# Performance work log

Hardware: AMD Instinct MI355X
Metric: run time of the kernel (lower is better)

## Reference

```python
import jax, jax.numpy as jnp
import numpy as np

EPS_LN = 1e-12
EPS_BN = 1e-5


def layernorm(x, w, b):
    u = jnp.mean(x, axis=-1, keepdims=True)
    s = jnp.mean((x - u) ** 2, axis=-1, keepdims=True)
    return w * ((x - u) / jnp.sqrt(s + EPS_LN)) + b


def reps_block(x, ln1_w, ln1_b, lin_w, lin_b, ln2_w, ln2_b):
    # GRAPHLayerNorm -> (dropout, identity in eval) -> Linear -> ReLU -> GRAPHLayerNorm
    h = layernorm(x, ln1_w, ln1_b)
    h = jax.nn.relu(jnp.einsum('bnd,od->bno', h, lin_w) + lin_b)
    return layernorm(h, ln2_w, ln2_b)


def attend(x):
    # full dense self-attention: softmax(x x^T) x ; dropout is identity in eval
    scores = jnp.einsum('bnd,bmd->bnm', x, x)  # [B,4096,4096]
    attn = jax.nn.softmax(scores, axis=-1)
    return jnp.einsum('bnm,bmd->bnd', attn, x)


def setup_inputs() -> dict:
    key = jax.random.key(0)
    ks = jax.random.split(key, 8)
    B, C, H, W = 4, 512, 64, 64
    D = 512
    inp = {
        'T1': jax.random.normal(ks[0], (B, C, H, W), jnp.float32),
        'T2': jax.random.normal(ks[1], (B, C, H, W), jnp.float32),
        'w_conv3': jax.random.normal(ks[2], (1024, 1024, 3, 3), jnp.float32) * 0.01,
        'w_conv1': jax.random.normal(ks[3], (512, 1024, 1, 1), jnp.float32) * 0.03,
        'bn_gamma': jnp.ones((512,), jnp.float32),
        'bn_beta': jnp.zeros((512,), jnp.float32),
        'bn_mean': jnp.zeros((512,), jnp.float32),
        'bn_var': jnp.ones((512,), jnp.float32),
        'ln1_w': jnp.ones((D,), jnp.float32),
        'ln1_b': jnp.zeros((D,), jnp.float32),
        'lin_w': jax.random.normal(ks[4], (D, D), jnp.float32) * 0.04,
        'lin_b': jnp.zeros((D,), jnp.float32),
        'ln2_w': jnp.ones((D,), jnp.float32),
        'ln2_b': jnp.zeros((D,), jnp.float32),
    }
    return inp


def reference(T1, T2, w_conv3, w_conv1, bn_gamma, bn_beta, bn_mean, bn_var,
              ln1_w, ln1_b, lin_w, lin_b, ln2_w, ln2_b):
    B = T1.shape[0]
    X = jnp.concatenate((T1, T2), axis=1)  # [B,1024,64,64]
    dn = ('NCHW', 'OIHW', 'NCHW')
    X = jax.lax.conv_general_dilated(X, w_conv3, (1, 1), ((1, 1), (1, 1)), dimension_numbers=dn)
    X = jax.lax.conv_general_dilated(X, w_conv1, (1, 1), ((0, 0), (0, 0)), dimension_numbers=dn)  # [B,512,64,64]
    # BatchNorm (eval, running stats) + ReLU
    inv = (bn_gamma / jnp.sqrt(bn_var + EPS_BN))[None, :, None, None]
    X = jax.nn.relu(X * inv + (bn_beta - bn_mean * bn_gamma / jnp.sqrt(bn_var + EPS_BN))[None, :, None, None])
    x = X.transpose(0, 2, 3, 1).reshape(B, 4096, 512)
    # block 1
    rel = attend(x)
    rel = reps_block(x + rel, ln1_w, ln1_b, lin_w, lin_b, ln2_w, ln2_b)
    # block 2 (original code reuses self.reps_graph, i.e. SAME params)
    rel1 = attend(rel)
    rel1 = reps_block(rel + rel1, ln1_w, ln1_b, lin_w, lin_b, ln2_w, ln2_b)
    return rel1.reshape(B, 64, 64, 512).transpose(0, 3, 1, 2)  # [B,512,64,64]
```

## Files before the change

kernel.cpp:

```cpp
#include <hip/hip_runtime.h>
#include <stdint.h>

typedef float f32x4 __attribute__((ext_vector_type(4)));
typedef __bf16 bf16x8 __attribute__((ext_vector_type(8)));
typedef unsigned short u16;
typedef unsigned short u16x8 __attribute__((ext_vector_type(8)));

__device__ __forceinline__ float bf2f(u16 u){ unsigned int i = ((unsigned int)u)<<16; float f; __builtin_memcpy(&f,&i,4); return f; }
__device__ __forceinline__ u16 f2bf(float f){ unsigned int i; __builtin_memcpy(&i,&f,4); i += 0x7FFFu + ((i>>16)&1u); return (u16)(i>>16); }
__device__ __forceinline__ u16 f2h(float f){ _Float16 h = (_Float16)f; u16 b; __builtin_memcpy(&b,&h,2); return b; }
__device__ __forceinline__ float h2f(u16 b){ _Float16 h; __builtin_memcpy(&h,&b,2); return (float)h; }

__device__ __forceinline__ void gld16(const void* g, void* l){
  __builtin_amdgcn_global_load_lds(
      (const __attribute__((address_space(1))) void*)(uintptr_t)g,
      (__attribute__((address_space(3))) void*)(unsigned int)(uintptr_t)l, 16, 0, 0);
}

__global__ __launch_bounds__(256) void pad_interior(const float* __restrict__ T1,
                                                    const float* __restrict__ T2,
                                                    u16* __restrict__ Xpad){
  const int n = blockIdx.z, ct = blockIdx.y, pt = blockIdx.x;
  const int t = threadIdx.x;
  const int c0 = ct*64, p0 = pt*64;
  const float* src = (c0 < 512) ? (T1 + ((long)n*512 + c0)*4096)
                                : (T2 + ((long)n*512 + (c0-512))*4096);
  __shared__ u16 lds[64][66];
  #pragma unroll
  for (int i=0;i<4;i++){
    int c = i*16 + (t>>4);
    int ch = t&15;
    float4 v = *(const float4*)(src + (long)c*4096 + p0 + ch*4);
    int p = ch*4;
    lds[p+0][c] = f2bf(v.x); lds[p+1][c] = f2bf(v.y);
    lds[p+2][c] = f2bf(v.z); lds[p+3][c] = f2bf(v.w);
  }
  __syncthreads();
  #pragma unroll
  for (int i=0;i<8;i++){
    int p = i*8 + (t>>5);
    int c2 = t&31;
    int pix = p0 + p; int yy = (pix>>6)+1, xx = (pix&63)+1;
    ushort2 val; val.x = lds[p][2*c2]; val.y = lds[p][2*c2+1];
    *(ushort2*)(Xpad + (((long)n*66 + yy)*66 + xx)*1024 + c0 + 2*c2) = val;
  }
}

__global__ __launch_bounds__(256) void prep_w3(const float* __restrict__ w3, u16* __restrict__ wk3t){
  const int o = blockIdx.x; const int t = threadIdx.x;
  __shared__ u16 lds[9216];
  const float* src = w3 + (long)o*9216;
  #pragma unroll
  for (int i=0;i<9;i++){
    int j = i*256 + t;
    float4 v = *(const float4*)(src + j*4);
    lds[j*4+0]=f2bf(v.x); lds[j*4+1]=f2bf(v.y); lds[j*4+2]=f2bf(v.z); lds[j*4+3]=f2bf(v.w);
  }
  __syncthreads();
  u16* dst = wk3t + (long)o*9216;
  #pragma unroll
  for (int i=0;i<36;i++){
    int j = i*256 + t; int tp = j>>10, ci = j&1023;
    dst[j] = lds[ci*9+tp];
  }
}

__global__ void prep_small(const float* __restrict__ w1, const float* __restrict__ bg,
                           const float* __restrict__ bb, const float* __restrict__ bm,
                           const float* __restrict__ bv, const float* __restrict__ linw,
                           u16* __restrict__ w1t, u16* __restrict__ lint,
                           float* __restrict__ bias1){
  const int b = blockIdx.x, t = threadIdx.x;
  if (b < 2048){
    long i = (long)b*256 + t;
    int o = (int)(i>>10);
    float inv = bg[o] / sqrtf(bv[o] + 1e-5f);
    w1t[i] = f2bf(w1[i]*inv);
  } else if (b < 3072){
    long i = (long)(b-2048)*256 + t;
    lint[i] = f2bf(linw[i]);
  } else {
    int o = (b-3072)*256 + t;
    float inv = bg[o]/sqrtf(bv[o]+1e-5f);
    bias1[o] = bb[o] - bm[o]*inv;
  }
}

__global__ __launch_bounds__(256) void row_norm(const u16* __restrict__ x, float* __restrict__ nrm){
  const int row = blockIdx.x*4 + (threadIdx.x>>6);
  const int lane = threadIdx.x & 63;
  u16x8 q = *(const u16x8*)(x + (long)row*512 + lane*8);
  float s = 0.f;
  #pragma unroll
  for (int j=0;j<8;j++){ float f = bf2f(q[j]); s += f*f; }
  #pragma unroll
  for (int off=32; off; off>>=1) s += __shfl_xor(s, off);
  if (lane==0) nrm[row] = s;
}

__global__ __launch_bounds__(256) void transpose_bf(const u16* __restrict__ src, u16* __restrict__ dst,
                                                    int R, int C, long sStr, long dStr){
  const int z = blockIdx.z;
  src += (long)z*sStr; dst += (long)z*dStr;
  const int r0 = blockIdx.x*64, c0 = blockIdx.y*64;
  const int t = threadIdx.x;
  __shared__ u16 lds[64][66];
  #pragma unroll
  for (int i=0;i<4;i++){
    int r = i*16 + (t>>4), ch = t&15;
    ushort4 v = *(const ushort4*)(src + (long)(r0+r)*C + c0 + ch*4);
    lds[r][ch*4+0]=v.x; lds[r][ch*4+1]=v.y; lds[r][ch*4+2]=v.z; lds[r][ch*4+3]=v.w;
  }
  __syncthreads();
  #pragma unroll
  for (int i=0;i<4;i++){
    int c = i*16 + (t>>4), ch = t&15;
    ushort4 v;
    v.x = lds[ch*4+0][c]; v.y = lds[ch*4+1][c]; v.z = lds[ch*4+2][c]; v.w = lds[ch*4+3][c];
    *(ushort4*)(dst + (long)(c0+c)*R + r0 + ch*4) = v;
  }
}

__global__ __launch_bounds__(256) void transpose_bf_f32(const u16* __restrict__ src, float* __restrict__ dst){
  const int z = blockIdx.z;
  src += (long)z*4096*512; dst += (long)z*512*4096;
  const int r0 = blockIdx.x*64, c0 = blockIdx.y*64;
  const int t = threadIdx.x;
  __shared__ u16 lds[64][66];
  #pragma unroll
  for (int i=0;i<4;i++){
    int r = i*16 + (t>>4), ch = t&15;
    ushort4 v = *(const ushort4*)(src + (long)(r0+r)*512 + c0 + ch*4);
    lds[r][ch*4+0]=v.x; lds[r][ch*4+1]=v.y; lds[r][ch*4+2]=v.z; lds[r][ch*4+3]=v.w;
  }
  __syncthreads();
  #pragma unroll
  for (int i=0;i<4;i++){
    int c = i*16 + (t>>4), ch = t&15;
    float4 v;
    v.x = bf2f(lds[ch*4+0][c]); v.y = bf2f(lds[ch*4+1][c]);
    v.z = bf2f(lds[ch*4+2][c]); v.w = bf2f(lds[ch*4+3][c]);
    *(float4*)(dst + (long)(c0+c)*4096 + r0 + ch*4) = v;
  }
}

template<int EPI, int CONV>
__global__ __launch_bounds__(512, 2) void gemm256(
    const u16* __restrict__ Ain, const u16* __restrict__ Btin, void* __restrict__ Cv,
    int K, int lda, int ldb, int ldc, const float* __restrict__ srowIn,
    u16* __restrict__ C0, u16* __restrict__ C1, u16* __restrict__ C2, u16* __restrict__ C3)
{
  extern __shared__ u16 sm[];
  const int t = threadIdx.x;
  const int lane = t & 63;
  const int wid = t >> 6;
  const int wr = wid >> 2, wc = wid & 3;

  long m0, n0;
  int byv = 0, bxv = 0;
  const u16* A; const u16* Bt; const float* srow; u16* Cz;
  if (EPI == 3){
    const int orig = blockIdx.x;
    const int swz = (orig & 7) * 68 + (orig >> 3);
    const int z = swz / 136;
    int p = swz % 136;
    int by = 0;
    while (p >= 16 - by){ p -= 16 - by; by++; }
    const int bx = by + p;
    byv = by; bxv = bx;
    m0 = (long)by * 256; n0 = (long)bx * 256;
    A = Ain + (long)z*4096*lda;
    Bt = A;
    srow = srowIn + (long)z*4096;
    Cz = (z==0)?C0:(z==1)?C1:(z==2)?C2:C3;
  } else {
    const int orig = blockIdx.y * gridDim.x + blockIdx.x;
    const int cpx = (gridDim.x * gridDim.y) >> 3;
    const int swz = (orig & 7) * cpx + (orig >> 3);
    const int bx = swz % gridDim.x;
    const int by = swz / gridDim.x;
    m0 = (long)by * 256; n0 = (long)bx * 256;
    A = Ain; Bt = Btin; srow = srowIn; Cz = (u16*)Cv;
  }

  const int row0 = t >> 2;
  const int cs0  = (t & 3) ^ ((row0 >> 1) & 3);

  const u16 *aB0, *aB1;
  if (CONV) {
    long m_ = m0 + row0;
    long pb0 = ((long)((int)(m_>>12)*66 + (int)((m_>>6)&63)))*66 + (int)(m_&63);
    m_ = m0 + row0 + 128;
    long pb1 = ((long)((int)(m_>>12)*66 + (int)((m_>>6)&63)))*66 + (int)(m_&63);
    aB0 = A + pb0*1024 + cs0*8;
    aB1 = A + pb1*1024 + cs0*8;
  } else {
    aB0 = A + (m0 + row0)*(long)lda + cs0*8;
    aB1 = A + (m0 + row0 + 128)*(long)lda + cs0*8;
  }
  const u16* bB0 = Bt + (n0 + row0)*(long)ldb + cs0*8;
  const u16* bB1 = Bt + (n0 + row0 + 128)*(long)ldb + cs0*8;

  auto issueA = [&](int sub, long aoff){
    u16* d = sm + sub*8192 + t*8;
    gld16(aB0 + aoff, d);
    gld16(aB1 + aoff, d + 4096);
  };
  auto issueB = [&](int sub, long boff){
    u16* d = sm + 32768 + sub*8192 + t*8;
    gld16(bB0 + boff, d);
    gld16(bB1 + boff, d + 4096);
  };
  auto conv_aoff = [&](int tile)->long {
    int kb = tile << 6;
    int tap = kb >> 10;
    int cb  = kb & 1023;
    int ky = (tap >= 6) ? 2 : (tap >= 3 ? 1 : 0);
    int kx = tap - ky*3;
    return (long)(ky*66 + kx)*1024 + cb;
  };

  const int frow = lane & 15;
  const int elemoff = (((lane>>4) ^ ((frow>>1)&3)) << 3);
  const int rAoff = (wr*128 + frow)*32 + elemoff;
  const int rBoff = (wc*64  + frow)*32 + elemoff;

  f32x4 acc[8][4] = {};

  {
    long a0 = CONV ? conv_aoff(0) : 0L;
    issueA(0, a0);
    issueB(0, 0);
    issueA(1, a0 + 32);
    issueB(1, 32);
  }

  const int NT = K >> 6;
  for (int tile = 0; tile < NT; ++tile) {
    const int b = tile & 1;
    const int nb2 = b ^ 1;
    const bool lastT = (tile == NT-1);
    long aoffN = 0, boffN = 0;
    if (!lastT) {
      aoffN = CONV ? conv_aoff(tile+1) : (long)(tile+1)*64;
      boffN = (long)(tile+1)*64;
    }

    asm volatile("s_waitcnt vmcnt(4)" ::: "memory");
    __builtin_amdgcn_s_barrier();
    __builtin_amdgcn_sched_barrier(0);

    {
      const u16* pA = sm + (b*2+0)*8192 + rAoff;
      const u16* pB = sm + 32768 + (b*2+0)*8192 + rBoff;
      bf16x8 bf[4];
      #pragma unroll
      for (int i=0;i<4;i++) bf[i] = *(const bf16x8*)(pB + i*512);
      {
        bf16x8 a[4];
        #pragma unroll
        for (int i=0;i<4;i++) a[i] = *(const bf16x8*)(pA + i*512);
        if (!lastT) issueA(nb2*2+0, aoffN);
        __builtin_amdgcn_s_setprio(1);
        #pragma unroll
        for (int mi=0;mi<4;mi++)
          #pragma unroll
          for (int ni=0;ni<4;ni++)
            acc[mi][ni] = __builtin_amdgcn_mfma_f32_16x16x32_bf16(a[mi], bf[ni], acc[mi][ni],0,0,0);
        __builtin_amdgcn_s_setprio(0);
      }
      {
        bf16x8 a[4];
        #pragma unroll
        for (int i=0;i<4;i++) a[i] = *(const bf16x8*)(pA + (4+i)*512);
        if (!lastT) issueB(nb2*2+0, boffN);
        __builtin_amdgcn_s_setprio(1);
        #pragma unroll
        for (int mi=0;mi<4;mi++)
          #pragma unroll
          for (int ni=0;ni<4;ni++)
            acc[4+mi][ni] = __builtin_amdgcn_mfma_f32_16x16x32_bf16(a[mi], bf[ni], acc[4+mi][ni],0,0,0);
        __builtin_amdgcn_s_setprio(0);
      }
    }

    if (lastT) asm volatile("s_waitcnt vmcnt(0)" ::: "memory");
    else       asm volatile("s_waitcnt vmcnt(4)" ::: "memory");
    __builtin_amdgcn_s_barrier();
    __builtin_amdgcn_sched_barrier(0);

    {
      const u16* pA = sm + (b*2+1)*8192 + rAoff;
      const u16* pB = sm + 32768 + (b*2+1)*8192 + rBoff;
      bf16x8 bf[4];
      #pragma unroll
      for (int i=0;i<4;i++) bf[i] = *(const bf16x8*)(pB + i*512);
      {
        bf16x8 a[4];
        #pragma unroll
        for (int i=0;i<4;i++) a[i] = *(const bf16x8*)(pA + i*512);
        if (!lastT) issueA(nb2*2+1, aoffN + 32);
        __builtin_amdgcn_s_setprio(1);
        #pragma unroll
        for (int mi=0;mi<4;mi++)
          #pragma unroll
          for (int ni=0;ni<4;ni++)
            acc[mi][ni] = __builtin_amdgcn_mfma_f32_16x16x32_bf16(a[mi], bf[ni], acc[mi][ni],0,0,0);
        __builtin_amdgcn_s_setprio(0);
      }
      {
        bf16x8 a[4];
        #pragma unroll
        for (int i=0;i<4;i++) a[i] = *(const bf16x8*)(pA + (4+i)*512);
        if (!lastT) issueB(nb2*2+1, boffN + 32);
        __builtin_amdgcn_s_setprio(1);
        #pragma unroll
        for (int mi=0;mi<4;mi++)
          #pragma unroll
          for (int ni=0;ni<4;ni++)
            acc[4+mi][ni] = __builtin_amdgcn_mfma_f32_16x16x32_bf16(a[mi], bf[ni], acc[4+mi][ni],0,0,0);
        __builtin_amdgcn_s_setprio(0);
      }
    }
  }

  const int crow0 = wr*128 + ((lane>>4)<<2);
  const int ccol0 = wc*64 + frow;

  #pragma unroll
  for (int mi=0;mi<8;mi++){
    #pragma unroll
    for (int ni=0;ni<4;ni++){
      long col = n0 + ccol0 + ni*16;
      #pragma unroll
      for (int r=0;r<4;r++){
        long row = m0 + crow0 + mi*16 + r;
        float v = acc[mi][ni][r];
        if (EPI==3) Cz[row*(long)ldc + col] = f2h(v - srow[row]);
        else        Cz[row*(long)ldc + col] = f2bf(v);
      }
    }
  }

  if (EPI == 3 && bxv != byv){
    __syncthreads();
    u16* lt = sm;
    float sc[4];
    #pragma unroll
    for (int ni=0;ni<4;ni++) sc[ni] = srow[n0 + ccol0 + ni*16];
    #pragma unroll
    for (int mi=0;mi<8;mi++){
      const int g = (crow0 + mi*16) >> 2;
      #pragma unroll
      for (int ni=0;ni<4;ni++){
        const int col_l = ccol0 + ni*16;
        ushort4 pk;
        #pragma unroll
        for (int r=0;r<4;r++) pk[r] = f2h(acc[mi][ni][r] - sc[ni]);
        *(ushort4*)(lt + col_l*256 + ((g ^ (col_l & 63))<<2)) = pk;
      }
    }
    __syncthreads();
    const int half = lane >> 5, l32 = lane & 31;
    #pragma unroll
    for (int ps=0; ps<16; ps++){
      const int R = ps*16 + wid*2 + half;
      const int u0 = ((l32<<1)    ) ^ (R & 63);
      const int u1 = ((l32<<1) | 1) ^ (R & 63);
      ushort4 a = *(const ushort4*)(lt + R*256 + (u0<<2));
      ushort4 b = *(const ushort4*)(lt + R*256 + (u1<<2));
      u16* dst = Cz + (n0 + R)*(long)ldc + m0 + (l32<<3);
      *(ushort4*)dst = a;
      *(ushort4*)(dst+4) = b;
    }
  }
}

template<int EPI>
__global__ __launch_bounds__(256, 2) void gemm_bt(
    const u16* __restrict__ A, const u16* __restrict__ Bt,
    void* __restrict__ Cv, const float* __restrict__ bias,
    int K, int lda, int ldb, int ldc)
{
  const int t = threadIdx.x;
  const int lane = t & 63;
  const int w = t >> 6;
  const int wr = w >> 1, wc = w & 1;
  const long m0 = (long)blockIdx.y * 128;
  const long n0 = (long)blockIdx.x * 128;

  __shared__ u16 lA[128*32];
  __shared__ u16 lB[128*32];

  const u16* aS0 = A + (m0 + (t>>2))*(long)lda + (t&3)*8;
  const u16* aS1 = aS0 + 64*(long)lda;
  const u16* bS0 = Bt + (n0 + (t>>2))*(long)ldb + (t&3)*8;
  const u16* bS1 = bS0 + 64*(long)ldb;
  u16* dA0 = lA + t*8; u16* dA1 = lA + 2048 + t*8;
  u16* dB0 = lB + t*8; u16* dB1 = lB + 2048 + t*8;

  f32x4 acc[4][4] = {};
  const int frow = lane & 15, kq = (lane >> 4) * 8;
  const u16* rA = lA + (wr*64 + frow)*32 + kq;
  const u16* rB = lB + (wc*64 + frow)*32 + kq;

  for (int kb = 0; kb < K; kb += 32) {
    gld16(aS0 + kb, dA0); gld16(aS1 + kb, dA1);
    gld16(bS0 + kb, dB0); gld16(bS1 + kb, dB1);
    __syncthreads();
    bf16x8 af[4], bfr[4];
    #pragma unroll
    for (int i=0;i<4;i++) af[i]  = *(const bf16x8*)(rA + i*512);
    #pragma unroll
    for (int i=0;i<4;i++) bfr[i] = *(const bf16x8*)(rB + i*512);
    #pragma unroll
    for (int mi=0;mi<4;mi++)
      #pragma unroll
      for (int ni=0;ni<4;ni++)
        acc[mi][ni] = __builtin_amdgcn_mfma_f32_16x16x32_bf16(af[mi], bfr[ni], acc[mi][ni], 0,0,0);
    __syncthreads();
  }

  const int crow0 = wr*64 + ((lane>>4)<<2);
  const int ccol0 = wc*64 + (lane&15);
  #pragma unroll
  for (int mi=0;mi<4;mi++){
    #pragma unroll
    for (int ni=0;ni<4;ni++){
      long col = n0 + ccol0 + ni*16;
      float bv = (EPI==1) ? bias[col] : 0.0f;
      #pragma unroll
      for (int r=0;r<4;r++){
        long row = m0 + crow0 + mi*16 + r;
        float v = acc[mi][ni][r];
        if (EPI==1){ v += bv; v = v > 0.0f ? v : 0.0f; }
        ((u16*)Cv)[row*(long)ldc + col] = f2bf(v);
      }
    }
  }
}

__global__ __launch_bounds__(256, 2) void pv5(
    const u16* __restrict__ P0, const u16* __restrict__ P1,
    const u16* __restrict__ P2, const u16* __restrict__ P3,
    const u16* __restrict__ xT, u16* __restrict__ attb)
{
  extern __shared__ u16 pm[];
  const int L = blockIdx.x;
  const int xcd = L & 7;
  const int z = xcd >> 1;
  const int tile = ((L >> 3) << 1) + (xcd & 1);
  const int bx = tile & 3, by = tile >> 2;
  const long ZS = 4096L*512;
  const u16* A  = (z==0)?P0:(z==1)?P1:(z==2)?P2:P3;
  const u16* Bt = xT   + (long)z*ZS;
  u16*       C  = attb + (long)z*ZS;
  const long m0 = (long)by * 128, n0 = (long)bx * 128;

  const int t = threadIdx.x;
  const int lane = t & 63;
  const int w = t >> 6;
  const int wr = w >> 1, wc = w & 1;

  const int row0 = t >> 2;
  const int cs0  = (t & 3) ^ ((row0 >> 1) & 3);

  const u16* aB0 = A + (m0 + row0)*4096L + cs0*8;
  const u16* aB1 = aB0 + 64*4096L;
  const u16* bB0 = Bt + (n0 + row0)*4096L + cs0*8;
  const u16* bB1 = bB0 + 64*4096L;

  auto issueA = [&](int sub, long off){
    u16* d = pm + sub*4096 + t*8;
    gld16(aB0 + off, d);
    gld16(aB1 + off, d + 2048);
  };
  auto issueB = [&](int sub, long off){
    u16* d = pm + 16384 + sub*4096 + t*8;
    gld16(bB0 + off, d);
    gld16(bB1 + off, d + 2048);
  };

  const int frow = lane & 15;
  const int elemoff = (((lane>>4) ^ ((frow>>1)&3)) << 3);
  const int rAoff = (wr*64 + frow)*32 + elemoff;
  const int rBoff = (wc*64 + frow)*32 + elemoff;

  f32x4 acc[4][4] = {};

  issueA(0, 0);  issueB(0, 0);
  issueA(1, 32); issueB(1, 32);

  const int NT = 64;
  for (int tl = 0; tl < NT; ++tl) {
    const int b = tl & 1;
    const int nb2 = b ^ 1;
    const bool lastT = (tl == NT-1);
    const long offN = (long)(tl+1)*64;

    asm volatile("s_waitcnt vmcnt(4)" ::: "memory");
    __builtin_amdgcn_s_barrier();
    __builtin_amdgcn_sched_barrier(0);

    {
      const u16* pA = pm + (b*2+0)*4096 + rAoff;
      const u16* pB = pm + 16384 + (b*2+0)*4096 + rBoff;
      bf16x8 bf[4];
      #pragma unroll
      for (int i=0;i<4;i++) bf[i] = *(const bf16x8*)(pB + i*512);
      {
        bf16x8 a[2];
        #pragma unroll
        for (int i=0;i<2;i++) a[i] = *(const bf16x8*)(pA + i*512);
        if (!lastT) issueA(nb2*2+0, offN);
        __builtin_amdgcn_s_setprio(1);
        #pragma unroll
        for (int mi=0;mi<2;mi++)
          #pragma unroll
          for (int ni=0;ni<4;ni++)
            acc[mi][ni] = __builtin_amdgcn_mfma_f32_16x16x32_bf16(a[mi], bf[ni], acc[mi][ni],0,0,0);
        __builtin_amdgcn_s_setprio(0);
      }
      {
        bf16x8 a[2];
        #pragma unroll
        for (int i=0;i<2;i++) a[i] = *(const bf16x8*)(pA + (2+i)*512);
        if (!lastT) issueB(nb2*2+0, offN);
        __builtin_amdgcn_s_setprio(1);
        #pragma unroll
        for (int mi=0;mi<2;mi++)
          #pragma unroll
          for (int ni=0;ni<4;ni++)
            acc[2+mi][ni] = __builtin_amdgcn_mfma_f32_16x16x32_bf16(a[mi], bf[ni], acc[2+mi][ni],0,0,0);
        __builtin_amdgcn_s_setprio(0);
      }
    }

    if (lastT) asm volatile("s_waitcnt vmcnt(0)" ::: "memory");
    else       asm volatile("s_waitcnt vmcnt(4)" ::: "memory");
    __builtin_amdgcn_s_barrier();
    __builtin_amdgcn_sched_barrier(0);

    {
      const u16* pA = pm + (b*2+1)*4096 + rAoff;
      const u16* pB = pm + 16384 + (b*2+1)*4096 + rBoff;
      bf16x8 bf[4];
      #pragma unroll
      for (int i=0;i<4;i++) bf[i] = *(const bf16x8*)(pB + i*512);
      {
        bf16x8 a[2];
        #pragma unroll
        for (int i=0;i<2;i++) a[i] = *(const bf16x8*)(pA + i*512);
        if (!lastT) issueA(nb2*2+1, offN + 32);
        __builtin_amdgcn_s_setprio(1);
        #pragma unroll
        for (int mi=0;mi<2;mi++)
          #pragma unroll
          for (int ni=0;ni<4;ni++)
            acc[mi][ni] = __builtin_amdgcn_mfma_f32_16x16x32_bf16(a[mi], bf[ni], acc[mi][ni],0,0,0);
        __builtin_amdgcn_s_setprio(0);
      }
      {
        bf16x8 a[2];
        #pragma unroll
        for (int i=0;i<2;i++) a[i] = *(const bf16x8*)(pA + (2+i)*512);
        if (!lastT) issueB(nb2*2+1, offN + 32);
        __builtin_amdgcn_s_setprio(1);
        #pragma unroll
        for (int mi=0;mi<2;mi++)
          #pragma unroll
          for (int ni=0;ni<4;ni++)
            acc[2+mi][ni] = __builtin_amdgcn_mfma_f32_16x16x32_bf16(a[mi], bf[ni], acc[2+mi][ni],0,0,0);
        __builtin_amdgcn_s_setprio(0);
      }
    }
  }

  const int crow0 = wr*64 + ((lane>>4)<<2);
  const int ccol0 = wc*64 + frow;
  #pragma unroll
  for (int mi=0;mi<4;mi++){
    #pragma unroll
    for (int ni=0;ni<4;ni++){
      long col = n0 + ccol0 + ni*16;
      #pragma unroll
      for (int r=0;r<4;r++){
        long row = m0 + crow0 + mi*16 + r;
        C[row*512 + col] = f2bf(acc[mi][ni][r]);
      }
    }
  }
}

__global__ __launch_bounds__(256) void softmax_batched(
    u16* __restrict__ S0, u16* __restrict__ S1,
    u16* __restrict__ S2, u16* __restrict__ S3)
{
  const int z = blockIdx.x >> 12;
  const long row = blockIdx.x & 4095;
  u16* buf = (z==0)?S0:(z==1)?S1:(z==2)?S2:S3;
  u16* src = buf + row*4096;
  const int t = threadIdx.x, lane = t&63, w = t>>6;
  float v[16];
  #pragma unroll
  for (int i=0;i<2;i++){
    u16x8 q = *(const u16x8*)(src + t*16 + i*8);
    #pragma unroll
    for (int j=0;j<8;j++) v[i*8+j] = h2f(q[j]);
  }
  float mx = v[0];
  #pragma unroll
  for (int i=1;i<16;i++) mx = fmaxf(mx, v[i]);
  #pragma unroll
  for (int off=32; off; off>>=1) mx = fmaxf(mx, __shfl_xor(mx, off));
  __shared__ float red[4];
  if (lane==0) red[w] = mx;
  __syncthreads();
  mx = fmaxf(fmaxf(red[0],red[1]), fmaxf(red[2],red[3]));
  float sum = 0.0f;
  #pragma unroll
  for (int i=0;i<16;i++){ v[i] = __expf(v[i]-mx); sum += v[i]; }
  #pragma unroll
  for (int off=32; off; off>>=1) sum += __shfl_xor(sum, off);
  __shared__ float red2[4];
  if (lane==0) red2[w] = sum;
  __syncthreads();
  sum = red2[0]+red2[1]+red2[2]+red2[3];
  const float inv = 1.0f/sum;
  #pragma unroll
  for (int i=0;i<2;i++){
    u16x8 o;
    #pragma unroll
    for (int j=0;j<8;j++) o[j] = f2bf(v[i*8+j]*inv);
    *(u16x8*)(src + t*16 + i*8) = o;
  }
}

template<int ADD>
__global__ __launch_bounds__(256) void ln_row(
    const u16* __restrict__ X, const u16* __restrict__ Y,
    const float* __restrict__ w, const float* __restrict__ b,
    u16* __restrict__ outB)
{
  const long row = blockIdx.x;
  const int t = threadIdx.x, lane = t&63, wv = t>>6;
  ushort2 xv = *(const ushort2*)(X + row*512 + t*2);
  float v0 = bf2f(xv.x), v1 = bf2f(xv.y);
  if (ADD){
    ushort2 yv = *(const ushort2*)(Y + row*512 + t*2);
    v0 += bf2f(yv.x); v1 += bf2f(yv.y);
  }
  float s = v0+v1, q = v0*v0 + v1*v1;
  #pragma unroll
  for (int off=32; off; off>>=1){ s += __shfl_xor(s,off); q += __shfl_xor(q,off); }
  __shared__ float red[8];
  if (lane==0){ red[wv]=s; red[4+wv]=q; }
  __syncthreads();
  s = red[0]+red[1]+red[2]+red[3];
  q = red[4]+red[5]+red[6]+red[7];
  const float u = s*(1.0f/512.0f);
  const float var = q*(1.0f/512.0f) - u*u;
  const float inv = rsqrtf(var + 1e-12f);
  const int c = t*2;
  float o0 = (v0-u)*inv*w[c]   + b[c];
  float o1 = (v1-u)*inv*w[c+1] + b[c+1];
  ushort2 ov; ov.x=f2bf(o0); ov.y=f2bf(o1);
  *(ushort2*)(outB + row*512 + c) = ov;
}

extern "C" void kernel_launch(void* const* d_in, const int* in_sizes, int n_in,
                              void* d_out, int out_size, void* d_ws, size_t ws_size,
                              hipStream_t stream) {
  const float* T1   = (const float*)d_in[0];
  const float* T2   = (const float*)d_in[1];
  const float* w3   = (const float*)d_in[2];
  const float* w1   = (const float*)d_in[3];
  const float* bg   = (const float*)d_in[4];
  const float* bb   = (const float*)d_in[5];
  const float* bm   = (const float*)d_in[6];
  const float* bv   = (const float*)d_in[7];
  const float* ln1w = (const float*)d_in[8];
  const float* ln1b = (const float*)d_in[9];
  const float* linw = (const float*)d_in[10];
  const float* linb = (const float*)d_in[11];
  const float* ln2w = (const float*)d_in[12];
  const float* ln2b = (const float*)d_in[13];

  hipFuncSetAttribute(reinterpret_cast<const void*>(gemm256<0,1>),
                      hipFuncAttributeMaxDynamicSharedMemorySize, 131072);
  hipFuncSetAttribute(reinterpret_cast<const void*>(gemm256<3,0>),
                      hipFuncAttributeMaxDynamicSharedMemorySize, 131072);
  hipFuncSetAttribute(reinterpret_cast<const void*>(pv5),
                      hipFuncAttributeMaxDynamicSharedMemorySize, 65536);

  char* ws = (char*)d_ws;
  size_t off = 0;
  auto alloc = [&](size_t bytes)->char* {
    char* p = ws + off;
    off += (bytes + 255) & ~(size_t)255;
    return p;
  };
  const size_t XPAD_B = 4L*66*66*1024*2;
  u16*   Xpad  = (u16*)  alloc(XPAD_B);
  u16*   wk3t  = (u16*)  alloc(1024L*9216*2);
  u16*   w1t   = (u16*)  alloc(512L*1024*2);
  u16*   lint  = (u16*)  alloc(512L*512*2);
  float* bias1 = (float*)alloc(512*4);
  float* nrm   = (float*)alloc(16384L*4);
  u16*   Y1    = (u16*)  alloc(16384L*1024*2);
  u16*   x0    = (u16*)  alloc(16384L*512*2);
  u16*   xT    = (u16*)  alloc(4L*512*4096*2);
  u16*   Sreg  = (u16*)  alloc(2L*4096*4096*2);
  u16*   attb  = (u16*)  alloc(16384L*512*2);
  u16*   h     = (u16*)  alloc(16384L*512*2);
  u16*   g     = (u16*)  alloc(16384L*512*2);
  u16*   rel1  = (u16*)  alloc(16384L*512*2);
  u16*   S0    = Y1;
  u16*   S1    = Sreg;
  u16*   S2    = Sreg + 4096L*4096;
  u16*   S3    = Xpad;
  if (off > ws_size) return;

  const long ZS = 4096L*512;

  hipMemsetAsync(Xpad, 0, XPAD_B, stream);
  pad_interior<<<dim3(64,16,4), 256, 0, stream>>>(T1, T2, Xpad);
  prep_w3<<<1024, 256, 0, stream>>>(w3, wk3t);
  prep_small<<<3074, 256, 0, stream>>>(w1, bg, bb, bm, bv, linw, w1t, lint, bias1);

  gemm256<0,1><<<dim3(4,64), 512, 131072, stream>>>(Xpad, wk3t, (void*)Y1, 9216, 0, 9216, 1024,
                                                    nullptr, nullptr, nullptr, nullptr, nullptr);
  gemm_bt<1><<<dim3(4,128), 256, 0, stream>>>(Y1, w1t, (void*)x0, bias1, 1024, 1024, 1024, 512);

  auto attend = [&](const u16* xin){
    transpose_bf<<<dim3(64,8,4), 256, 0, stream>>>(xin, xT, 4096, 512, ZS, ZS);
    row_norm<<<4096, 256, 0, stream>>>(xin, nrm);
    gemm256<3,0><<<dim3(544), 512, 131072, stream>>>(xin, xin, nullptr, 512, 512, 512, 4096,
                                                     nrm, S0, S1, S2, S3);
    softmax_batched<<<16384, 256, 0, stream>>>(S0, S1, S2, S3);
    pv5<<<512, 256, 65536, stream>>>(S0, S1, S2, S3, xT, attb);
  };

  attend(x0);
  ln_row<1><<<16384, 256, 0, stream>>>(x0, attb, ln1w, ln1b, h);
  gemm_bt<1><<<dim3(4,128), 256, 0, stream>>>(h, lint, (void*)g, linb, 512, 512, 512, 512);
  ln_row<0><<<16384, 256, 0, stream>>>(g, nullptr, ln2w, ln2b, rel1);

  attend(rel1);
  ln_row<1><<<16384, 256, 0, stream>>>(rel1, attb, ln1w, ln1b, h);
  gemm_bt<1><<<dim3(4,128), 256, 0, stream>>>(h, lint, (void*)g, linb, 512, 512, 512, 512);
  ln_row<0><<<16384, 256, 0, stream>>>(g, nullptr, ln2w, ln2b, x0);

  transpose_bf_f32<<<dim3(64,8,4), 256, 0, stream>>>(x0, (float*)d_out);
}
```

Baseline: 814.5 us.

## Replace simple 128x128 GEMM with deep-pipelined swizzled LDS GEMM and XCD-aware tile mapping

Replaces the single-buffered gemm_bt, which synchronised twice per 32-wide K step, with gemm128_deep. The new kernel double-buffers two 32-wide K sub-tiles in dynamic LDS, issues the next loads between MFMA groups, and uses vmcnt waits with s_setprio. It also XOR-swizzles the LDS layout to reduce bank conflicts and remaps block indices so tiles are grouped per XCD for L2 locality. pv5's tile mapping is changed as well. The cost is more LDS per block (64KB), which may limit occupancy, and hand-scheduled waits that are fragile.

```diff
diff --git a/kernel.cpp b/kernel.cpp
--- a/kernel.cpp
+++ b/kernel.cpp
@@ -377,52 +377,139 @@
 }
 
 template<int EPI>
-__global__ __launch_bounds__(256, 2) void gemm_bt(
-    const u16* __restrict__ A, const u16* __restrict__ Bt,
-    void* __restrict__ Cv, const float* __restrict__ bias,
-    int K, int lda, int ldb, int ldc)
+__global__ __launch_bounds__(256, 2) void gemm128_deep(
+    const u16* __restrict__ A, const u16* __restrict__ Bt, u16* __restrict__ C,
+    const float* __restrict__ bias, int K, int lda, int ldb, int ldc)
 {
+  extern __shared__ u16 pm[];
+  const int L = blockIdx.x;
+  const int xcd = L & 7;
+  const int q = L >> 3;
+  const int by = (q >> 2) + xcd*16;
+  const int bx = q & 3;
+  const long m0 = (long)by * 128, n0 = (long)bx * 128;
+
   const int t = threadIdx.x;
   const int lane = t & 63;
   const int w = t >> 6;
   const int wr = w >> 1, wc = w & 1;
-  const long m0 = (long)blockIdx.y * 128;
-  const long n0 = (long)blockIdx.x * 128;
-
-  __shared__ u16 lA[128*32];
-  __shared__ u16 lB[128*32];
-
-  const u16* aS0 = A + (m0 + (t>>2))*(long)lda + (t&3)*8;
-  const u16* aS1 = aS0 + 64*(long)lda;
-  const u16* bS0 = Bt + (n0 + (t>>2))*(long)ldb + (t&3)*8;
-  const u16* bS1 = bS0 + 64*(long)ldb;
-  u16* dA0 = lA + t*8; u16* dA1 = lA + 2048 + t*8;
-  u16* dB0 = lB + t*8; u16* dB1 = lB + 2048 + t*8;
+
+  const int row0 = t >> 2;
+  const int cs0  = (t & 3) ^ ((row0 >> 1) & 3);
+
+  const u16* aB0 = A + (m0 + row0)*(long)lda + cs0*8;
+  const u16* aB1 = aB0 + 64*(long)lda;
+  const u16* bB0 = Bt + (n0 + row0)*(long)ldb + cs0*8;
+  const u16* bB1 = bB0 + 64*(long)ldb;
+
+  auto issueA = [&](int sub, long off){
+    u16* d = pm + sub*4096 + t*8;
+    gld16(aB0 + off, d);
+    gld16(aB1 + off, d + 2048);
+  };
+  auto issueB = [&](int sub, long off){
+    u16* d = pm + 16384 + sub*4096 + t*8;
+    gld16(bB0 + off, d);
+    gld16(bB1 + off, d + 2048);
+  };
+
+  const int frow = lane & 15;
+  const int elemoff = (((lane>>4) ^ ((frow>>1)&3)) << 3);
+  const int rAoff = (wr*64 + frow)*32 + elemoff;
+  const int rBoff = (wc*64 + frow)*32 + elemoff;
 
   f32x4 acc[4][4] = {};
-  const int frow = lane & 15, kq = (lane >> 4) * 8;
-  const u16* rA = lA + (wr*64 + frow)*32 + kq;
-  const u16* rB = lB + (wc*64 + frow)*32 + kq;
-
-  for (int kb = 0; kb < K; kb += 32) {
-    gld16(aS0 + kb, dA0); gld16(aS1 + kb, dA1);
-    gld16(bS0 + kb, dB0); gld16(bS1 + kb, dB1);
-    __syncthreads();
-    bf16x8 af[4], bfr[4];
-    #pragma unroll
-    for (int i=0;i<4;i++) af[i]  = *(const bf16x8*)(rA + i*512);
-    #pragma unroll
-    for (int i=0;i<4;i++) bfr[i] = *(const bf16x8*)(rB + i*512);
-    #pragma unroll
-    for (int mi=0;mi<4;mi++)
-      #pragma unroll
-      for (int ni=0;ni<4;ni++)
-        acc[mi][ni] = __builtin_amdgcn_mfma_f32_16x16x32_bf16(af[mi], bfr[ni], acc[mi][ni], 0,0,0);
-    __syncthreads();
+
+  issueA(0, 0);  issueB(0, 0);
+  issueA(1, 32); issueB(1, 32);
+
+  const int NT = K >> 6;
+  for (int tl = 0; tl < NT; ++tl) {
+    const int b = tl & 1;
+    const int nb2 = b ^ 1;
+    const bool lastT = (tl == NT-1);
+    const long offN = (long)(tl+1)*64;
+
+    asm volatile("s_waitcnt vmcnt(4)" ::: "memory");
+    __builtin_amdgcn_s_barrier();
+    __builtin_amdgcn_sched_barrier(0);
+
+    {
+      const u16* pA = pm + (b*2+0)*4096 + rAoff;
+      const u16* pB = pm + 16384 + (b*2+0)*4096 + rBoff;
+      bf16x8 bf[4];
+      #pragma unroll
+      for (int i=0;i<4;i++) bf[i] = *(const bf16x8*)(pB + i*512);
+      {
+        bf16x8 a[2];
+        #pragma unroll
+        for (int i=0;i<2;i++) a[i] = *(const bf16x8*)(pA + i*512);
+        if (!lastT) issueA(nb2*2+0, offN);
+        __builtin_amdgcn_s_setprio(1);
+        #pragma unroll
+        for (int mi=0;mi<2;mi++)
+          #pragma unroll
+          for (int ni=0;ni<4;ni++)
+            acc[mi][ni] = __builtin_amdgcn_mfma_f32_16x16x32_bf16(a[mi], bf[ni], acc[mi][ni],0,0,0);
+        __builtin_amdgcn_s_setprio(0);
+      }
+      {
+        bf16x8 a[2];
+        #pragma unroll
+        for (int i=0;i<2;i++) a[i] = *(const bf16x8*)(pA + (2+i)*512);
+        if (!lastT) issueB(nb2*2+0, offN);
+        __builtin_amdgcn_s_setprio(1);
+        #pragma unroll
+        for (int mi=0;mi<2;mi++)
+          #pragma unroll
+          for (int ni=0;ni<4;ni++)
+            acc[2+mi][ni] = __builtin_amdgcn_mfma_f32_16x16x32_bf16(a[mi], bf[ni], acc[2+mi][ni],0,0,0);
+        __builtin_amdgcn_s_setprio(0);
+      }
+    }
+
+    if (lastT) asm volatile("s_waitcnt vmcnt(0)" ::: "memory");
+    else       asm volatile("s_waitcnt vmcnt(4)" ::: "memory");
+    __builtin_amdgcn_s_barrier();
+    __builtin_amdgcn_sched_barrier(0);
+
+    {
+      const u16* pA = pm + (b*2+1)*4096 + rAoff;
+      const u16* pB = pm + 16384 + (b*2+1)*4096 + rBoff;
+      bf16x8 bf[4];
+      #pragma unroll
+      for (int i=0;i<4;i++) bf[i] = *(const bf16x8*)(pB + i*512);
+      {
+        bf16x8 a[2];
+        #pragma unroll
+        for (int i=0;i<2;i++) a[i] = *(const bf16x8*)(pA + i*512);
+        if (!lastT) issueA(nb2*2+1, offN + 32);
+        __builtin_amdgcn_s_setprio(1);
+        #pragma unroll
+        for (int mi=0;mi<2;mi++)
+          #pragma unroll
+          for (int ni=0;ni<4;ni++)
+            acc[mi][ni] = __builtin_amdgcn_mfma_f32_16x16x32_bf16(a[mi], bf[ni], acc[mi][ni],0,0,0);
+        __builtin_amdgcn_s_setprio(0);
+      }
+      {
+        bf16x8 a[2];
+        #pragma unroll
+        for (int i=0;i<2;i++) a[i] = *(const bf16x8*)(pA + (2+i)*512);
+        if (!lastT) issueB(nb2*2+1, offN + 32);
+        __builtin_amdgcn_s_setprio(1);
+        #pragma unroll
+        for (int mi=0;mi<2;mi++)
+          #pragma unroll
+          for (int ni=0;ni<4;ni++)
+            acc[2+mi][ni] = __builtin_amdgcn_mfma_f32_16x16x32_bf16(a[mi], bf[ni], acc[2+mi][ni],0,0,0);
+        __builtin_amdgcn_s_setprio(0);
+      }
+    }
   }
 
   const int crow0 = wr*64 + ((lane>>4)<<2);
-  const int ccol0 = wc*64 + (lane&15);
+  const int ccol0 = wc*64 + frow;
   #pragma unroll
   for (int mi=0;mi<4;mi++){
     #pragma unroll
@@ -434,7 +521,7 @@
         long row = m0 + crow0 + mi*16 + r;
         float v = acc[mi][ni][r];
         if (EPI==1){ v += bv; v = v > 0.0f ? v : 0.0f; }
-        ((u16*)Cv)[row*(long)ldc + col] = f2bf(v);
+        C[row*(long)ldc + col] = f2bf(v);
       }
     }
   }
@@ -449,8 +536,9 @@
   const int L = blockIdx.x;
   const int xcd = L & 7;
   const int z = xcd >> 1;
-  const int tile = ((L >> 3) << 1) + (xcd & 1);
-  const int bx = tile & 3, by = tile >> 2;
+  const int q = L >> 3;
+  const int by = ((q >> 2) << 1) + (xcd & 1);
+  const int bx = q & 3;
   const long ZS = 4096L*512;
   const u16* A  = (z==0)?P0:(z==1)?P1:(z==2)?P2:P3;
   const u16* Bt = xT   + (long)z*ZS;
@@ -691,6 +779,10 @@
   hipFuncSetAttribute(reinterpret_cast<const void*>(gemm256<3,0>),
                       hipFuncAttributeMaxDynamicSharedMemorySize, 131072);
   hipFuncSetAttribute(reinterpret_cast<const void*>(pv5),
+                      hipFuncAttributeMaxDynamicSharedMemorySize, 65536);
+  hipFuncSetAttribute(reinterpret_cast<const void*>(gemm128_deep<0>),
+                      hipFuncAttributeMaxDynamicSharedMemorySize, 65536);
+  hipFuncSetAttribute(reinterpret_cast<const void*>(gemm128_deep<1>),
                       hipFuncAttributeMaxDynamicSharedMemorySize, 65536);
 
   char* ws = (char*)d_ws;
@@ -730,7 +822,7 @@
 
   gemm256<0,1><<<dim3(4,64), 512, 131072, stream>>>(Xpad, wk3t, (void*)Y1, 9216, 0, 9216, 1024,
                                                     nullptr, nullptr, nullptr, nullptr, nullptr);
-  gemm_bt<1><<<dim3(4,128), 256, 0, stream>>>(Y1, w1t, (void*)x0, bias1, 1024, 1024, 1024, 512);
+  gemm128_deep<1><<<512, 256, 65536, stream>>>(Y1, w1t, x0, bias1, 1024, 1024, 1024, 512);
 
   auto attend = [&](const u16* xin){
     transpose_bf<<<dim3(64,8,4), 256, 0, stream>>>(xin, xT, 4096, 512, ZS, ZS);
@@ -743,12 +835,12 @@
 
   attend(x0);
   ln_row<1><<<16384, 256, 0, stream>>>(x0, attb, ln1w, ln1b, h);
-  gemm_bt<1><<<dim3(4,128), 256, 0, stream>>>(h, lint, (void*)g, linb, 512, 512, 512, 512);
+  gemm128_deep<1><<<512, 256, 65536, stream>>>(h, lint, g, linb, 512, 512, 512, 512);
   ln_row<0><<<16384, 256, 0, stream>>>(g, nullptr, ln2w, ln2b, rel1);
 
   attend(rel1);
   ln_row<1><<<16384, 256, 0, stream>>>(rel1, attb, ln1w, ln1b, h);
-  gemm_bt<1><<<dim3(4,128), 256, 0, stream>>>(h, lint, (void*)g, linb, 512, 512, 512, 512);
+  gemm128_deep<1><<<512, 256, 65536, stream>>>(h, lint, g, linb, 512, 512, 512, 512);
   ln_row<0><<<16384, 256, 0, stream>>>(g, nullptr, ln2w, ln2b, x0);
 
   transpose_bf_f32<<<dim3(64,8,4), 256, 0, stream>>>(x0, (float*)d_out);
```

Result: faster. 796.8 us (-2.2%).
